# Kernel optimization log

Hardware: AMD Instinct MI355X
Metric: run time of the kernel (lower is better)

The kernel has to match this reference:

```python
import jax, jax.numpy as jnp
import numpy as np
import math

EMBED_DIM = 128
N_HEADS = 8
HEAD_DIM = EMBED_DIM // N_HEADS
VEH_FEAT = 5
TANH_CLIP = 10.0


def setup_inputs() -> dict:
    key = jax.random.key(0)
    ks = jax.random.split(key, 12)
    b, v, E = 8192, 64, EMBED_DIM
    s = 1.0 / math.sqrt(E)
    return {
        "graph_embedding": jax.random.normal(ks[0], (b, E), jnp.float32),
        "vehicle_features": jax.random.normal(ks[1], (b, v, VEH_FEAT), jnp.float32),
        "vehicle_location_emb": jax.random.normal(ks[2], (b, v, E), jnp.float32),
        "mask": jax.random.randint(ks[3], (b, v), 0, 2) > 0,
        # vehicle_proj: Linear(5+E -> E)
        "Wvp": jax.random.uniform(ks[4], (E, VEH_FEAT + E), jnp.float32, -s, s),
        "bvp": jax.random.uniform(ks[5], (E,), jnp.float32, -s, s),
        # MultiheadAttention packed in-proj (q,k,v) and out-proj
        "in_proj_w": jax.random.uniform(ks[6], (3 * E, E), jnp.float32, -s, s),
        "in_proj_b": jnp.zeros((3 * E,), jnp.float32),
        "out_w": jax.random.uniform(ks[7], (E, E), jnp.float32, -s, s),
        "out_b": jnp.zeros((E,), jnp.float32),
        # pointer projections (no bias)
        "Wq2": jax.random.uniform(ks[8], (E, E), jnp.float32, -s, s),
        "Wk2": jax.random.uniform(ks[9], (E, E), jnp.float32, -s, s),
    }


def reference(graph_embedding, vehicle_features, vehicle_location_emb, mask,
              Wvp, bvp, in_proj_w, in_proj_b, out_w, out_b, Wq2, Wk2):
    b, v, _ = vehicle_features.shape
    E, H, D = EMBED_DIM, N_HEADS, HEAD_DIM

    # vehicle_proj on concat([features, location_emb])
    full = jnp.concatenate([vehicle_features, vehicle_location_emb], axis=-1)  # [b,v,5+E]
    h = full @ Wvp.T + bvp                                                      # [b,v,E]

    # MultiheadAttention: single-token query = graph embedding
    Wq, Wk, Wv = jnp.split(in_proj_w, 3, axis=0)
    bq, bk, bv_ = jnp.split(in_proj_b, 3, axis=0)
    qp = (graph_embedding @ Wq.T + bq).reshape(b, 1, H, D)  # [b,1,H,D]
    kp = (h @ Wk.T + bk).reshape(b, v, H, D)                # [b,v,H,D]
    vp = (h @ Wv.T + bv_).reshape(b, v, H, D)

    scores = jnp.einsum("bqhd,bkhd->bhqk", qp, kp) / math.sqrt(D)  # [b,H,1,v]
    scores = jnp.where(mask[:, None, None, :], -jnp.inf, scores)
    attn = jax.nn.softmax(scores, axis=-1)
    ctx = jnp.einsum("bhqk,bkhd->bqhd", attn, vp).reshape(b, 1, E)
    attended = ctx @ out_w.T + out_b                                # [b,1,E]

    # pointer logits + tanh clipping + mask
    q2 = attended @ Wq2.T            # [b,1,E]
    k2 = h @ Wk2.T                   # [b,v,E]
    logits = jnp.einsum("bqe,bve->bv", q2, k2) / math.sqrt(E)
    logits = TANH_CLIP * jnp.tanh(logits)
    return jnp.where(mask, -jnp.inf, logits)
```

## Files before the change

### kernel.cpp

```cpp
#include <hip/hip_runtime.h>
#include <hip/hip_bf16.h>
#include <math.h>

#define V     64
#define E     128
#define NH    8
#define HD    16
#define CF    5
#define K133  133
#define PITCH 132

#define NEG_BIG (-3.0e38f)

typedef __attribute__((ext_vector_type(8))) short bf16x8;
typedef __attribute__((ext_vector_type(4))) float f32x4;

static __device__ __forceinline__ short f2bf(float f) {
    __hip_bfloat16 h = __float2bfloat16(f);
    return *reinterpret_cast<short*>(&h);
}

__global__ __launch_bounds__(256, 3)
void vsd_kernel(const float* __restrict__ ge,
                const float* __restrict__ feat,
                const float* __restrict__ loc,
                const unsigned char* __restrict__ maskp,
                const float* __restrict__ Wvp,
                const float* __restrict__ bvp,
                const float* __restrict__ ipw,
                const float* __restrict__ ipb,
                const float* __restrict__ outw,
                const float* __restrict__ outb,
                const float* __restrict__ Wq2,
                const float* __restrict__ Wk2,
                float* __restrict__ out)
{
    __shared__ float sH[V * PITCH];
    __shared__ float sAux[2560];
    __shared__ float sFeat[V * 8];
    __shared__ float sGe[E];
    __shared__ float sQp[E];
    __shared__ float sQb[NH];
    __shared__ float sCtx[E];
    __shared__ float sAtt[E];
    __shared__ float sQ2[E];
    __shared__ float sR[E];
    __shared__ int   sMask[V];
    __shared__ int   sBad;

    const int i    = blockIdx.x;
    const int t    = threadIdx.x;
    const int lane = t & 63;
    const int w    = t >> 6;

    float* sSvec = sAux;
    float* sU    = sAux + 1024;
    float* sScor = sAux + 2048;

    const float* fbase = feat + (size_t)i * V * CF;
    const float* locB  = loc  + (size_t)i * V * E;

    if (t == 0) sBad = 0;
    {
        int j = t / 5, c = t - 5 * j;
        sFeat[j * 8 + c] = fbase[t];
        if (t < 64) {
            int tt = t + 256;
            int j2 = tt / 5, c2 = tt - 5 * j2;
            sFeat[j2 * 8 + c2] = fbase[tt];
        }
        if (t < E) sGe[t] = ge[(size_t)i * E + t];
        if (t < V) sMask[t] = maskp[(size_t)i * V + t];
    }
    __syncthreads();

    {
        const int l15 = lane & 15, l4 = lane >> 4;
        f32x4 acc[4][2];
        #pragma unroll
        for (int jt = 0; jt < 4; ++jt)
            #pragma unroll
            for (int cbl = 0; cbl < 2; ++cbl) {
                acc[jt][cbl][0] = 0.f; acc[jt][cbl][1] = 0.f;
                acc[jt][cbl][2] = 0.f; acc[jt][cbl][3] = 0.f;
            }

        #pragma unroll
        for (int kb = 0; kb < 4; ++kb) {
            bf16x8 afr[4];
            #pragma unroll
            for (int jt = 0; jt < 4; ++jt) {
                const float* ap = locB + (size_t)(16 * jt + l15) * E + 32 * kb + 8 * l4;
                float4 x = *(const float4*)ap;
                float4 y = *(const float4*)(ap + 4);
                bf16x8 a;
                a[0] = f2bf(x.x); a[1] = f2bf(x.y); a[2] = f2bf(x.z); a[3] = f2bf(x.w);
                a[4] = f2bf(y.x); a[5] = f2bf(y.y); a[6] = f2bf(y.z); a[7] = f2bf(y.w);
                afr[jt] = a;
            }
            #pragma unroll
            for (int cbl = 0; cbl < 2; ++cbl) {
                const int e = 32 * w + 16 * cbl + l15;
                const float* wp = Wvp + (size_t)e * K133 + CF + 32 * kb + 8 * l4;
                bf16x8 b;
                #pragma unroll
                for (int jj = 0; jj < 8; ++jj) b[jj] = f2bf(wp[jj]);
                #pragma unroll
                for (int jt = 0; jt < 4; ++jt)
                    acc[jt][cbl] = __builtin_amdgcn_mfma_f32_16x16x32_bf16(
                        afr[jt], b, acc[jt][cbl], 0, 0, 0);
            }
        }

        #pragma unroll
        for (int cbl = 0; cbl < 2; ++cbl) {
            const int e = 32 * w + 16 * cbl + l15;
            const float* wr = Wvp + (size_t)e * K133;
            const float w0 = wr[0], w1 = wr[1], w2 = wr[2], w3 = wr[3], w4 = wr[4];
            const float bias = bvp[e];
            #pragma unroll
            for (int jt = 0; jt < 4; ++jt) {
                #pragma unroll
                for (int r = 0; r < 4; ++r) {
                    const int j = 16 * jt + 4 * l4 + r;
                    const float* fj = &sFeat[j * 8];
                    float vv = acc[jt][cbl][r] + bias;
                    vv = fmaf(fj[0], w0, vv);
                    vv = fmaf(fj[1], w1, vv);
                    vv = fmaf(fj[2], w2, vv);
                    vv = fmaf(fj[3], w3, vv);
                    vv = fmaf(fj[4], w4, vv);
                    sH[j * PITCH + e] = vv;
                }
            }
        }
    }
    __syncthreads();

    if (i == 0) {
        const int j = t & 63;
        const int e = ((t >> 6) * 32) + (t & 31);
        float a = bvp[e];
        #pragma unroll
        for (int c = 0; c < CF; ++c)
            a = fmaf(fbase[j * CF + c], Wvp[(size_t)e * K133 + c], a);
        for (int k = 0; k < E; ++k)
            a = fmaf(locB[j * E + k], Wvp[(size_t)e * K133 + CF + k], a);
        if (fabsf(a - sH[j * PITCH + e]) > 0.25f) sBad = 1;
    }

    if (t < E) {
        const int e = t;
        const float* wrow = ipw + (size_t)e * E;
        float a = ipb[e];
        #pragma unroll
        for (int c = 0; c < E; c += 4) {
            float4 w4 = *(const float4*)&wrow[c];
            a = fmaf(w4.x, sGe[c],     a);
            a = fmaf(w4.y, sGe[c + 1], a);
            a = fmaf(w4.z, sGe[c + 2], a);
            a = fmaf(w4.w, sGe[c + 3], a);
        }
        sQp[e] = a;
    }
    __syncthreads();

    {
        #pragma unroll
        for (int m = 0; m < 4; ++m) {
            int idx = t + 256 * m;
            int h8 = idx >> 7, c = idx & 127;
            const float* wk = ipw + (size_t)E * E + (size_t)(h8 * HD) * E + c;
            float a = 0.f;
            #pragma unroll
            for (int d = 0; d < HD; ++d)
                a = fmaf(sQp[h8 * HD + d], wk[(size_t)d * E], a);
            sSvec[idx] = a;
        }
        if (t < NH) {
            const float* bk = ipb + E;
            float a = 0.f;
            #pragma unroll
            for (int d = 0; d < HD; ++d)
                a = fmaf(sQp[t * HD + d], bk[t * HD + d], a);
            sQb[t] = a;
        }
    }
    __syncthreads();

    {
        #pragma unroll
        for (int m = 0; m < 2; ++m) {
            int idx = t + 256 * m;
            int h8 = idx >> 6, k = idx & 63;
            const float* hv = &sH[k * PITCH];
            const float* sv = &sSvec[h8 * E];
            float a = sQb[h8];
            #pragma unroll
            for (int c = 0; c < E; c += 4) {
                float4 h4 = *(const float4*)&hv[c];
                a = fmaf(h4.x, sv[c],     a);
                a = fmaf(h4.y, sv[c + 1], a);
                a = fmaf(h4.z, sv[c + 2], a);
                a = fmaf(h4.w, sv[c + 3], a);
            }
            a *= 0.25f;
            if (sMask[k]) a = -INFINITY;
            sScor[h8 * 64 + k] = a;
        }
    }
    __syncthreads();

    {
        #pragma unroll
        for (int rep = 0; rep < 2; ++rep) {
            int h8 = w + 4 * rep;
            float x = sScor[h8 * 64 + lane];
            float mx = x;
            #pragma unroll
            for (int off = 32; off; off >>= 1)
                mx = fmaxf(mx, __shfl_xor(mx, off, 64));
            float p = expf(x - mx);
            float s = p;
            #pragma unroll
            for (int off = 32; off; off >>= 1)
                s += __shfl_xor(s, off, 64);
            sScor[h8 * 64 + lane] = p / s;
        }
    }
    __syncthreads();

    {
        #pragma unroll
        for (int m = 0; m < 4; ++m) {
            int idx = t + 256 * m;
            int h8 = idx >> 7, c = idx & 127;
            const float* att = &sScor[h8 * 64];
            float a = 0.f;
            #pragma unroll 8
            for (int k = 0; k < V; ++k)
                a = fmaf(att[k], sH[k * PITCH + c], a);
            sU[h8 * E + c] = a;
        }
    }
    __syncthreads();

    if (t < E) {
        const int e = t, h8 = e >> 4;
        const float* wv = ipw + (size_t)2 * E * E + (size_t)e * E;
        const float* uu = &sU[h8 * E];
        float a = ipb[2 * E + e];
        #pragma unroll
        for (int c = 0; c < E; c += 4) {
            float4 w4 = *(const float4*)&wv[c];
            a = fmaf(w4.x, uu[c],     a);
            a = fmaf(w4.y, uu[c + 1], a);
            a = fmaf(w4.z, uu[c + 2], a);
            a = fmaf(w4.w, uu[c + 3], a);
        }
        sCtx[e] = a;
    }
    __syncthreads();

    if (t < E) {
        const int e = t;
        const float* wv = outw + (size_t)e * E;
        float a = outb[e];
        #pragma unroll
        for (int c = 0; c < E; c += 4) {
            float4 w4 = *(const float4*)&wv[c];
            a = fmaf(w4.x, sCtx[c],     a);
            a = fmaf(w4.y, sCtx[c + 1], a);
            a = fmaf(w4.z, sCtx[c + 2], a);
            a = fmaf(w4.w, sCtx[c + 3], a);
        }
        sAtt[e] = a;
    }
    __syncthreads();

    if (t < E) {
        const int e = t;
        const float* wv = Wq2 + (size_t)e * E;
        float a = 0.f;
        #pragma unroll
        for (int c = 0; c < E; c += 4) {
            float4 w4 = *(const float4*)&wv[c];
            a = fmaf(w4.x, sAtt[c],     a);
            a = fmaf(w4.y, sAtt[c + 1], a);
            a = fmaf(w4.z, sAtt[c + 2], a);
            a = fmaf(w4.w, sAtt[c + 3], a);
        }
        sQ2[e] = a;
    }
    __syncthreads();

    if (t < E) {
        const int c = t;
        float a = 0.f;
        #pragma unroll 8
        for (int ee = 0; ee < E; ++ee)
            a = fmaf(sQ2[ee], Wk2[(size_t)ee * E + c], a);
        sR[c] = a;
    }
    __syncthreads();

    if (t < V) {
        const int k = t;
        const float* hv = &sH[k * PITCH];
        float a = 0.f;
        #pragma unroll
        for (int c = 0; c < E; c += 4) {
            float4 h4 = *(const float4*)&hv[c];
            a = fmaf(h4.x, sR[c],     a);
            a = fmaf(h4.y, sR[c + 1], a);
            a = fmaf(h4.z, sR[c + 2], a);
            a = fmaf(h4.w, sR[c + 3], a);
        }
        float lg = a * 0.088388347648318447f;
        out[(size_t)i * V + k] = sMask[k] ? NEG_BIG : 10.0f * tanhf(lg);
    }

    if (i == 0 && t < V) {
        if (sBad) out[t] = __builtin_nanf("");
    }
}

extern "C" void kernel_launch(void* const* d_in, const int* in_sizes, int n_in,
                              void* d_out, int out_size, void* d_ws, size_t ws_size,
                              hipStream_t stream) {
    const float* ge    = (const float*)d_in[0];
    const float* feat  = (const float*)d_in[1];
    const float* loc   = (const float*)d_in[2];
    const unsigned char* mask = (const unsigned char*)d_in[3];
    const float* Wvp   = (const float*)d_in[4];
    const float* bvp   = (const float*)d_in[5];
    const float* ipw   = (const float*)d_in[6];
    const float* ipb   = (const float*)d_in[7];
    const float* outw  = (const float*)d_in[8];
    const float* outb  = (const float*)d_in[9];
    const float* Wq2   = (const float*)d_in[10];
    const float* Wk2   = (const float*)d_in[11];
    float* out = (float*)d_out;

    const int B = in_sizes[0] / E;
    vsd_kernel<<<B, 256, 0, stream>>>(ge, feat, loc, mask, Wvp, bvp, ipw, ipb,
                                      outw, outb, Wq2, Wk2, out);
}
```

Measured before the change: 1.171 ms.

## Stage location embeddings once into swizzled LDS as bf16 before MFMA

Each 64x128 location-embedding tile is now loaded once, cooperatively by all four waves, converted to bf16 and written into an XOR-swizzled shared buffer. The MFMA loop then reads its A fragments from LDS. Previously every wave reloaded the whole tile from global memory and converted it itself, which is four times redundant. To fit the new 16 KB staging buffer, the small shared vectors are aliased onto two buffers and the LDS union is enlarged. This may lower occupancy, and the aliasing is only safe if the phase lifetimes truly do not overlap.

```diff
diff --git a/kernel.cpp b/kernel.cpp
--- a/kernel.cpp
+++ b/kernel.cpp
@@ -36,15 +36,11 @@
                 float* __restrict__ out)
 {
     __shared__ float sH[V * PITCH];
-    __shared__ float sAux[2560];
+    __shared__ __align__(16) char sUnion[16384];
     __shared__ float sFeat[V * 8];
-    __shared__ float sGe[E];
-    __shared__ float sQp[E];
+    __shared__ float sSmallA[E];
+    __shared__ float sSmallB[E];
     __shared__ float sQb[NH];
-    __shared__ float sCtx[E];
-    __shared__ float sAtt[E];
-    __shared__ float sQ2[E];
-    __shared__ float sR[E];
     __shared__ int   sMask[V];
     __shared__ int   sBad;
 
@@ -53,15 +49,31 @@
     const int lane = t & 63;
     const int w    = t >> 6;
 
-    float* sSvec = sAux;
-    float* sU    = sAux + 1024;
-    float* sScor = sAux + 2048;
+    float* sSvec  = (float*)sUnion;
+    float* sU     = (float*)sUnion + 1024;
+    float* sScor  = (float*)sUnion + 2048;
+
+    float* sGe  = sSmallA;  float* sAtt = sSmallA;  float* sR  = sSmallA;
+    float* sQp  = sSmallB;  float* sCtx = sSmallB;  float* sQ2 = sSmallB;
 
     const float* fbase = feat + (size_t)i * V * CF;
     const float* locB  = loc  + (size_t)i * V * E;
 
     if (t == 0) sBad = 0;
     {
+        #pragma unroll
+        for (int m = 0; m < 4; ++m) {
+            int g  = t + 256 * m;
+            int j  = g >> 4, ch = g & 15;
+            const float* p = locB + j * 128 + ch * 8;
+            float4 x = *(const float4*)p;
+            float4 y = *(const float4*)(p + 4);
+            bf16x8 a;
+            a[0] = f2bf(x.x); a[1] = f2bf(x.y); a[2] = f2bf(x.z); a[3] = f2bf(x.w);
+            a[4] = f2bf(y.x); a[5] = f2bf(y.y); a[6] = f2bf(y.z); a[7] = f2bf(y.w);
+            int ch2 = ch ^ (j & 7);
+            *(bf16x8*)(sUnion + j * 256 + ch2 * 16) = a;
+        }
         int j = t / 5, c = t - 5 * j;
         sFeat[j * 8 + c] = fbase[t];
         if (t < 64) {
@@ -85,31 +97,29 @@
                 acc[jt][cbl][2] = 0.f; acc[jt][cbl][3] = 0.f;
             }
 
-        #pragma unroll
+        #pragma unroll 1
         for (int kb = 0; kb < 4; ++kb) {
-            bf16x8 afr[4];
-            #pragma unroll
-            for (int jt = 0; jt < 4; ++jt) {
-                const float* ap = locB + (size_t)(16 * jt + l15) * E + 32 * kb + 8 * l4;
-                float4 x = *(const float4*)ap;
-                float4 y = *(const float4*)(ap + 4);
-                bf16x8 a;
-                a[0] = f2bf(x.x); a[1] = f2bf(x.y); a[2] = f2bf(x.z); a[3] = f2bf(x.w);
-                a[4] = f2bf(y.x); a[5] = f2bf(y.y); a[6] = f2bf(y.z); a[7] = f2bf(y.w);
-                afr[jt] = a;
-            }
+            bf16x8 bfr[2];
             #pragma unroll
             for (int cbl = 0; cbl < 2; ++cbl) {
                 const int e = 32 * w + 16 * cbl + l15;
                 const float* wp = Wvp + (size_t)e * K133 + CF + 32 * kb + 8 * l4;
-                bf16x8 b;
                 #pragma unroll
-                for (int jj = 0; jj < 8; ++jj) b[jj] = f2bf(wp[jj]);
+                for (int jj = 0; jj < 8; ++jj) bfr[cbl][jj] = f2bf(wp[jj]);
+            }
+            bf16x8 afr[4];
+            #pragma unroll
+            for (int jt = 0; jt < 4; ++jt) {
+                const int r   = 16 * jt + l15;
+                const int ch2 = (4 * kb + l4) ^ (r & 7);
+                afr[jt] = *(const bf16x8*)(sUnion + r * 256 + ch2 * 16);
+            }
+            #pragma unroll
+            for (int cbl = 0; cbl < 2; ++cbl)
                 #pragma unroll
                 for (int jt = 0; jt < 4; ++jt)
                     acc[jt][cbl] = __builtin_amdgcn_mfma_f32_16x16x32_bf16(
-                        afr[jt], b, acc[jt][cbl], 0, 0, 0);
-            }
+                        afr[jt], bfr[cbl], acc[jt][cbl], 0, 0, 0);
         }
 
         #pragma unroll
```

After: 1.103 ms. -5.8%, faster.
